# Performance work log

Measured on AMD Instinct MI355X. Metric: run time of the kernel, lower is better.

The kernel has to match this reference:

```python
import jax, jax.numpy as jnp
import numpy as np

B, S, D = 8, 2048, 1024

def setup_inputs() -> dict:
    key = jax.random.key(0)
    ks = jax.random.split(key, 9)
    s = 1.0 / np.sqrt(D)
    return {
        "x": jax.random.normal(ks[0], (B, S, D), dtype=jnp.float32),
        "Wq": jax.random.uniform(ks[1], (D, D), jnp.float32, -s, s),
        "bq": jax.random.uniform(ks[2], (D,), jnp.float32, -s, s),
        "Wk": jax.random.uniform(ks[3], (D, D), jnp.float32, -s, s),
        "bk": jax.random.uniform(ks[4], (D,), jnp.float32, -s, s),
        "Wv": jax.random.uniform(ks[5], (D, D), jnp.float32, -s, s),
        "bv": jax.random.uniform(ks[6], (D,), jnp.float32, -s, s),
        "Wo": jax.random.uniform(ks[7], (D, 1), jnp.float32, -s, s),
        "bo": jax.random.uniform(ks[8], (1,), jnp.float32, -s, s),
    }

def reference(x, Wq, bq, Wk, bk, Wv, bv, Wo, bo):
    q = x @ Wq + bq                      # [B,S,D]
    k = x @ Wk + bk                      # [B,S,D]
    v = x @ Wv + bv                      # [B,S,D]
    scores = jnp.einsum('bsd,btd->bst', q, k)   # [B,S,S], NOTE: no 1/sqrt(D) scaling in source
    attn = jax.nn.softmax(scores, axis=-1)
    out = jnp.einsum('bst,btd->bsd', attn, v)   # [B,S,D]
    return out @ Wo + bo                 # [B,S,1]
```

## Files before the change

### kernel.cpp

```cpp
#include <hip/hip_runtime.h>
#include <stdint.h>

#define D_ 1024
#define S_ 2048
#define B_ 8

typedef _Float16 h16;
typedef _Float16 f16x8 __attribute__((ext_vector_type(8)));
typedef _Float16 f16x4 __attribute__((ext_vector_type(4)));
typedef float    f32x4 __attribute__((ext_vector_type(4)));

typedef __attribute__((address_space(3))) void lds_void;
typedef const __attribute__((address_space(1))) void g_void;

#define MFMA16(a, b, c) __builtin_amdgcn_mfma_f32_16x16x32_f16(a, b, c, 0, 0, 0)
#define VMCNT(n) asm volatile("s_waitcnt vmcnt(" #n ")" ::: "memory")
#define SFENCE() __builtin_amdgcn_sched_barrier(0)
#define SBAR() __builtin_amdgcn_s_barrier()

__device__ __forceinline__ void stage16(const h16* g0, int ld, h16* lchunk) {
  int lane = threadIdx.x & 63;
  int c = (lane & 3) ^ ((lane >> 3) & 3);
  const h16* ga = g0 + (size_t)(lane >> 2) * ld + c * 8;
  __builtin_amdgcn_global_load_lds((g_void*)ga, (lds_void*)lchunk, 16, 0, 0);
}

__global__ void k_cast(const float* __restrict__ Wq, const float* __restrict__ Wk,
                       h16* __restrict__ Wqh, h16* __restrict__ Wkh) {
  int i = blockIdx.x * 256 + threadIdx.x;
  const int n4 = (D_ * D_) / 4;
  const float4* src;
  h16* dst;
  if (i < n4) { src = (const float4*)Wq; dst = Wqh; }
  else        { src = (const float4*)Wk; dst = Wkh; i -= n4; }
  float4 a = src[i];
  f16x4 o;
  o[0] = (h16)a.x; o[1] = (h16)a.y; o[2] = (h16)a.z; o[3] = (h16)a.w;
  *(f16x4*)(dst + (size_t)i * 4) = o;
}

__global__ void k_u(const float* __restrict__ Wv, const float* __restrict__ Wk,
                    const float* __restrict__ Wo, const float* __restrict__ bq_,
                    const float* __restrict__ bv, float* __restrict__ u,
                    float* __restrict__ v2) {
  int lane = threadIdx.x & 63;
  if (blockIdx.x == 256) {
    if (threadIdx.x < 64) {
      float s = 0.f;
      #pragma unroll
      for (int j = 0; j < 4; ++j) {
        float4 a = ((const float4*)bv)[j * 64 + lane];
        float4 b = ((const float4*)Wo)[j * 64 + lane];
        s += a.x * b.x + a.y * b.y + a.z * b.z + a.w * b.w;
      }
      #pragma unroll
      for (int off = 32; off; off >>= 1) s += __shfl_xor(s, off, 64);
      if (lane == 0) u[D_] = s;
    }
    return;
  }
  int row = blockIdx.x * 4 + (threadIdx.x >> 6);
  const float4* rv = (const float4*)(Wv + (size_t)row * D_);
  const float4* rk = (const float4*)(Wk + (size_t)row * D_);
  const float4* w4 = (const float4*)Wo;
  const float4* b4 = (const float4*)bq_;
  float s1 = 0.f, s2 = 0.f;
  #pragma unroll
  for (int j = 0; j < 4; ++j) {
    int c = j * 64 + lane;
    float4 a = rv[c], b = w4[c];
    s1 += a.x * b.x + a.y * b.y + a.z * b.z + a.w * b.w;
    float4 e = rk[c], f = b4[c];
    s2 += e.x * f.x + e.y * f.y + e.z * f.z + e.w * f.w;
  }
  #pragma unroll
  for (int off = 32; off; off >>= 1) {
    s1 += __shfl_xor(s1, off, 64);
    s2 += __shfl_xor(s2, off, 64);
  }
  if (lane == 0) { u[row] = s1; v2[row] = s2; }
}

__global__ void k_xw(const float* __restrict__ x, const float* __restrict__ u,
                     const float* __restrict__ v2, h16* __restrict__ xh,
                     float* __restrict__ w, float* __restrict__ cv) {
  int row = blockIdx.x * 4 + (threadIdx.x >> 6);
  int lane = threadIdx.x & 63;
  const float4* xr = (const float4*)(x + (size_t)row * D_);
  const float4* u4 = (const float4*)u;
  const float4* c4 = (const float4*)v2;
  h16* xo = xh + (size_t)row * D_;
  float s1 = 0.f, s2 = 0.f;
  #pragma unroll
  for (int j = 0; j < 4; ++j) {
    int c = j * 64 + lane;
    float4 a = xr[c];
    float4 b = u4[c];
    float4 e = c4[c];
    s1 += a.x * b.x + a.y * b.y + a.z * b.z + a.w * b.w;
    s2 += a.x * e.x + a.y * e.y + a.z * e.z + a.w * e.w;
    f16x4 o;
    o[0] = (h16)a.x; o[1] = (h16)a.y; o[2] = (h16)a.z; o[3] = (h16)a.w;
    *(f16x4*)(xo + c * 4) = o;
  }
  #pragma unroll
  for (int off = 32; off; off >>= 1) {
    s1 += __shfl_xor(s1, off, 64);
    s2 += __shfl_xor(s2, off, 64);
  }
  if (lane == 0) { w[row] = s1 + u[D_]; cv[row] = s2; }
}

__global__ __launch_bounds__(256, 4) void k_mt(
    const h16* __restrict__ Wkh, const h16* __restrict__ Wqh,
    h16* __restrict__ Mt) {
  __shared__ alignas(16) h16 As[3][128 * 32];
  __shared__ alignas(16) h16 Bs[3][128 * 32];
  int tid = threadIdx.x;
  int w = tid >> 6, lane = tid & 63;
  int wr = w >> 1, wc = w & 1;
  int g = lane >> 4, l15 = lane & 15;
  int swz = (l15 >> 1) & 3;
  int m0 = (blockIdx.x >> 3) * 128, n0 = (blockIdx.x & 7) * 128;

  const h16* abase0 = Wkh + (size_t)(m0 + (2 * w) * 16) * D_;
  const h16* abase1 = abase0 + (size_t)16 * D_;
  const h16* bbase0 = Wqh + (size_t)(n0 + (2 * w) * 16) * D_;
  const h16* bbase1 = bbase0 + (size_t)16 * D_;

  f32x4 acc[4][4] = {};

  #define STAGE_MT(ap, bp, k)                                \
    {                                                        \
      int k0_ = (k) * 32;                                    \
      stage16(abase0 + k0_, D_, (ap) + (2 * w) * 512);       \
      stage16(abase1 + k0_, D_, (ap) + (2 * w + 1) * 512);   \
      stage16(bbase0 + k0_, D_, (bp) + (2 * w) * 512);       \
      stage16(bbase1 + k0_, D_, (bp) + (2 * w + 1) * 512);   \
    }

  h16 *A0 = As[0], *A1 = As[1], *A2 = As[2];
  h16 *B0 = Bs[0], *B1 = Bs[1], *B2 = Bs[2];
  STAGE_MT(A0, B0, 0);
  STAGE_MT(A1, B1, 1);
  for (int k = 0; k < 32; ++k) {
    if (k + 2 < 32) {
      STAGE_MT(A2, B2, k + 2);
      VMCNT(8);
    } else if (k + 1 < 32) {
      VMCNT(4);
    } else {
      VMCNT(0);
    }
    SFENCE();
    SBAR();
    SFENCE();
    f16x8 af[4], bf[4];
    #pragma unroll
    for (int i = 0; i < 4; ++i) {
      af[i] = *(const f16x8*)(A0 + (wr * 64 + i * 16 + l15) * 32 + (g ^ swz) * 8);
      bf[i] = *(const f16x8*)(B0 + (wc * 64 + i * 16 + l15) * 32 + (g ^ swz) * 8);
    }
    __builtin_amdgcn_s_setprio(1);
    #pragma unroll
    for (int mi = 0; mi < 4; ++mi)
      #pragma unroll
      for (int ni = 0; ni < 4; ++ni)
        acc[mi][ni] = MFMA16(af[mi], bf[ni], acc[mi][ni]);
    __builtin_amdgcn_s_setprio(0);
    SBAR();
    h16* t;
    t = A0; A0 = A1; A1 = A2; A2 = t;
    t = B0; B0 = B1; B1 = B2; B2 = t;
  }

  #pragma unroll
  for (int ni = 0; ni < 4; ++ni) {
    int n = n0 + wc * 64 + ni * 16 + l15;
    #pragma unroll
    for (int mi = 0; mi < 4; ++mi) {
      #pragma unroll
      for (int r = 0; r < 4; ++r) {
        int m = m0 + wr * 64 + mi * 16 + g * 4 + r;
        Mt[(size_t)m * D_ + n] = (h16)(acc[mi][ni][r]);
      }
    }
  }
}

__global__ __launch_bounds__(512, 4) void k_y(
    const h16* __restrict__ xh, const h16* __restrict__ Mt,
    h16* __restrict__ y) {
  __shared__ alignas(16) h16 As[3][256 * 32];
  __shared__ alignas(16) h16 Bs[3][128 * 32];
  int tid = threadIdx.x;
  int w = tid >> 6, lane = tid & 63;
  int wrow = w >> 1, wcol = w & 1;
  int g = lane >> 4, l15 = lane & 15;
  int swz = (l15 >> 1) & 3;

  int idx = (blockIdx.x & 7) * 64 + (blockIdx.x >> 3);
  int m0 = (idx >> 3) * 256, n0 = (idx & 7) * 128;

  const h16* abase0 = xh + (size_t)(m0 + (2 * w) * 16) * D_;
  const h16* abase1 = abase0 + (size_t)16 * D_;
  const h16* bbase  = Mt + (size_t)(n0 + w * 16) * D_;

  f32x4 acc[4][4] = {};

  #define STAGE_Y(ap, bp, k)                                 \
    {                                                        \
      int k0_ = (k) * 32;                                    \
      stage16(abase0 + k0_, D_, (ap) + (2 * w) * 512);       \
      stage16(abase1 + k0_, D_, (ap) + (2 * w + 1) * 512);   \
      stage16(bbase + k0_, D_, (bp) + w * 512);              \
    }

  h16 *A0 = As[0], *A1 = As[1], *A2 = As[2];
  h16 *B0 = Bs[0], *B1 = Bs[1], *B2 = Bs[2];
  STAGE_Y(A0, B0, 0);
  STAGE_Y(A1, B1, 1);
  for (int k = 0; k < 32; ++k) {
    if (k + 2 < 32) {
      STAGE_Y(A2, B2, k + 2);
      VMCNT(6);
    } else if (k + 1 < 32) {
      VMCNT(3);
    } else {
      VMCNT(0);
    }
    SFENCE();
    SBAR();
    SFENCE();
    f16x8 af[4], bf[4];
    #pragma unroll
    for (int i = 0; i < 4; ++i) {
      af[i] = *(const f16x8*)(A0 + (wrow * 64 + i * 16 + l15) * 32 + (g ^ swz) * 8);
      bf[i] = *(const f16x8*)(B0 + (wcol * 64 + i * 16 + l15) * 32 + (g ^ swz) * 8);
    }
    __builtin_amdgcn_s_setprio(1);
    #pragma unroll
    for (int mi = 0; mi < 4; ++mi)
      #pragma unroll
      for (int ni = 0; ni < 4; ++ni)
        acc[mi][ni] = MFMA16(af[mi], bf[ni], acc[mi][ni]);
    __builtin_amdgcn_s_setprio(0);
    SBAR();
    h16* t;
    t = A0; A0 = A1; A1 = A2; A2 = t;
    t = B0; B0 = B1; B1 = B2; B2 = t;
  }

  #pragma unroll
  for (int ni = 0; ni < 4; ++ni) {
    int n = n0 + wcol * 64 + ni * 16 + l15;
    #pragma unroll
    for (int mi = 0; mi < 4; ++mi) {
      #pragma unroll
      for (int r = 0; r < 4; ++r) {
        int m = m0 + wrow * 64 + mi * 16 + g * 4 + r;
        y[(size_t)m * D_ + n] = (h16)(acc[mi][ni][r]);
      }
    }
  }
}

__global__ __launch_bounds__(512, 4) void k_attn(
    const h16* __restrict__ y, const h16* __restrict__ xh,
    const float* __restrict__ wv, const float* __restrict__ cv,
    float* __restrict__ part) {
  __shared__ alignas(16) h16 Qs[3][128 * 32];
  __shared__ alignas(16) h16 Ks[3][256 * 32];
  __shared__ float sm[3][4][128];
  int tid = threadIdx.x;
  int w = tid >> 6, lane = tid & 63;
  int g = lane >> 4, l15 = lane & 15;
  int swz = (l15 >> 1) & 3;
  int wq = w >> 2, wkc = w & 3;
  int b = blockIdx.x & 7;
  int r = blockIdx.x >> 3;
  int kc = r >> 4;
  int q0 = (r & 15) * 128;
  size_t rbase = (size_t)b * S_;

  const h16* qbase  = y + (rbase + q0 + w * 16) * D_;
  const h16* kbase0 = xh + (rbase + kc * 256 + (2 * w) * 16) * D_;
  const h16* kbase1 = kbase0 + (size_t)16 * D_;

  #define STAGE_ATTN(qp, kp, st)                             \
    {                                                        \
      int k0_ = (st) * 32;                                   \
      stage16(qbase + k0_, D_, (qp) + w * 512);              \
      stage16(kbase0 + k0_, D_, (kp) + (2 * w) * 512);       \
      stage16(kbase1 + k0_, D_, (kp) + (2 * w + 1) * 512);   \
    }

  f32x4 acc[4][4] = {};

  h16 *Q0 = Qs[0], *Q1 = Qs[1], *Q2 = Qs[2];
  h16 *K0 = Ks[0], *K1 = Ks[1], *K2 = Ks[2];
  STAGE_ATTN(Q0, K0, 0);
  STAGE_ATTN(Q1, K1, 1);
  for (int st = 0; st < 32; ++st) {
    if (st + 2 < 32) {
      STAGE_ATTN(Q2, K2, st + 2);
      VMCNT(6);
    } else if (st + 1 < 32) {
      VMCNT(3);
    } else {
      VMCNT(0);
    }
    SFENCE();
    SBAR();
    SFENCE();
    f16x8 qf[4], kf[4];
    #pragma unroll
    for (int i = 0; i < 4; ++i) {
      qf[i] = *(const f16x8*)(Q0 + (wq * 64 + i * 16 + l15) * 32 + (g ^ swz) * 8);
      kf[i] = *(const f16x8*)(K0 + (wkc * 64 + i * 16 + l15) * 32 + (g ^ swz) * 8);
    }
    __builtin_amdgcn_s_setprio(1);
    #pragma unroll
    for (int mi = 0; mi < 4; ++mi)
      #pragma unroll
      for (int ni = 0; ni < 4; ++ni)
        acc[mi][ni] = MFMA16(qf[mi], kf[ni], acc[mi][ni]);
    __builtin_amdgcn_s_setprio(0);
    SBAR();
    h16* t;
    t = Q0; Q0 = Q1; Q1 = Q2; Q2 = t;
    t = K0; K0 = K1; K1 = K2; K2 = t;
  }

  float wvv[4], cvv[4];
  #pragma unroll
  for (int ni = 0; ni < 4; ++ni) {
    size_t t = rbase + kc * 256 + wkc * 64 + ni * 16 + l15;
    wvv[ni] = wv[t];
    cvv[ni] = cv[t];
  }
  #pragma unroll
  for (int mi = 0; mi < 4; ++mi) {
    #pragma unroll
    for (int rr = 0; rr < 4; ++rr) {
      float s0 = acc[mi][0][rr] + cvv[0];
      float s1 = acc[mi][1][rr] + cvv[1];
      float s2 = acc[mi][2][rr] + cvv[2];
      float s3 = acc[mi][3][rr] + cvv[3];
      float v = fmaxf(fmaxf(s0, s1), fmaxf(s2, s3));
      #pragma unroll
      for (int off = 1; off < 16; off <<= 1) v = fmaxf(v, __shfl_xor(v, off, 64));
      float p0 = __expf(s0 - v), p1 = __expf(s1 - v);
      float p2 = __expf(s2 - v), p3 = __expf(s3 - v);
      float pn = p0 * wvv[0] + p1 * wvv[1] + p2 * wvv[2] + p3 * wvv[3];
      float pd = p0 + p1 + p2 + p3;
      #pragma unroll
      for (int off = 1; off < 16; off <<= 1) {
        pn += __shfl_xor(pn, off, 64);
        pd += __shfl_xor(pd, off, 64);
      }
      if (l15 == 0) {
        int row = wq * 64 + mi * 16 + g * 4 + rr;
        sm[0][wkc][row] = v;
        sm[1][wkc][row] = pn;
        sm[2][wkc][row] = pd;
      }
    }
  }
  __syncthreads();
  if (tid < 128) {
    float M = sm[0][0][tid];
    #pragma unroll
    for (int j = 1; j < 4; ++j) M = fmaxf(M, sm[0][j][tid]);
    float N = 0.f, Dn = 0.f;
    #pragma unroll
    for (int j = 0; j < 4; ++j) {
      float e = __expf(sm[0][j][tid] - M);
      N += sm[1][j][tid] * e;
      Dn += sm[2][j][tid] * e;
    }
    size_t row = rbase + q0 + tid;
    part[row * 24 + kc * 3 + 0] = M;
    part[row * 24 + kc * 3 + 1] = N;
    part[row * 24 + kc * 3 + 2] = Dn;
  }
}

__global__ void k_fin(const float* __restrict__ part, const float* __restrict__ bo,
                      float* __restrict__ out) {
  int idx = blockIdx.x * 256 + threadIdx.x;
  if (idx >= B_ * S_) return;
  const float* p = part + (size_t)idx * 24;
  float M = p[0];
  #pragma unroll
  for (int j = 1; j < 8; ++j) M = fmaxf(M, p[j * 3]);
  float N = 0.f, Dn = 0.f;
  #pragma unroll
  for (int j = 0; j < 8; ++j) {
    float e = __expf(p[j * 3] - M);
    N += p[j * 3 + 1] * e;
    Dn += p[j * 3 + 2] * e;
  }
  out[idx] = N / Dn + bo[0];
}

extern "C" void kernel_launch(void* const* d_in, const int* in_sizes, int n_in,
                              void* d_out, int out_size, void* d_ws, size_t ws_size,
                              hipStream_t stream) {
  const float* x  = (const float*)d_in[0];
  const float* Wq = (const float*)d_in[1];
  const float* bq = (const float*)d_in[2];
  const float* Wk = (const float*)d_in[3];
  const float* bk = (const float*)d_in[4];
  const float* Wv = (const float*)d_in[5];
  const float* bv = (const float*)d_in[6];
  const float* Wo = (const float*)d_in[7];
  const float* bo = (const float*)d_in[8];
  float* out = (float*)d_out;
  (void)bk;

  char* ws = (char*)d_ws;
  h16*   xh   = (h16*)ws;
  h16*   yb   = (h16*)(ws + (size_t)32 * 1024 * 1024);
  h16*   Mt   = (h16*)(ws + (size_t)64 * 1024 * 1024);
  h16*   Wqh  = (h16*)(ws + (size_t)66 * 1024 * 1024);
  h16*   Wkh  = (h16*)(ws + (size_t)68 * 1024 * 1024);
  float* wv   = (float*)(ws + (size_t)70 * 1024 * 1024);
  float* cv   = (float*)(ws + (size_t)70 * 1024 * 1024 + 65536);
  float* u    = (float*)(ws + (size_t)70 * 1024 * 1024 + 131072);
  float* v2   = (float*)(ws + (size_t)70 * 1024 * 1024 + 139264);
  float* part = (float*)(ws + (size_t)71 * 1024 * 1024);

  hipLaunchKernelGGL(k_cast, dim3(2048), dim3(256), 0, stream, Wq, Wk, Wqh, Wkh);
  hipLaunchKernelGGL(k_u,    dim3(257),  dim3(256), 0, stream, Wv, Wk, Wo, bq, bv, u, v2);
  hipLaunchKernelGGL(k_xw,   dim3(4096), dim3(256), 0, stream, x, u, v2, xh, wv, cv);
  hipLaunchKernelGGL(k_mt,   dim3(64),   dim3(256), 0, stream, Wkh, Wqh, Mt);
  hipLaunchKernelGGL(k_y,    dim3(512),  dim3(512), 0, stream, xh, Mt, yb);
  hipLaunchKernelGGL(k_attn, dim3(1024), dim3(512), 0, stream, yb, xh, wv, cv, part);
  hipLaunchKernelGGL(k_fin,  dim3(64),   dim3(256), 0, stream, part, bo, out);
}
```

Baseline: 269.0 us.

## Enlarge GEMM tiles to 256x256 in y and attention-score kernels

Both the y-projection GEMM and the attention score GEMM move from 256x128 (128x256) block tiles to 256x256 tiles. Each wave now computes 128x64 with 8x4 MFMA accumulators, and grid sizes are halved. The aim is higher arithmetic intensity, fewer global and LDS loads per flop, and fewer blocks. The cost is more registers and LDS per block, with launch bounds lowered to 2 blocks per CU, which reduces occupancy and tail-wave balance across 256 CUs.

New measurement: 286.5 us. +6.5%, slower.

```diff
diff --git a/kernel.cpp b/kernel.cpp
--- a/kernel.cpp
+++ b/kernel.cpp
@@ -188,32 +188,34 @@
   }
 }
 
-__global__ __launch_bounds__(512, 4) void k_y(
+__global__ __launch_bounds__(512, 2) void k_y(
     const h16* __restrict__ xh, const h16* __restrict__ Mt,
     h16* __restrict__ y) {
   __shared__ alignas(16) h16 As[3][256 * 32];
-  __shared__ alignas(16) h16 Bs[3][128 * 32];
+  __shared__ alignas(16) h16 Bs[3][256 * 32];
   int tid = threadIdx.x;
   int w = tid >> 6, lane = tid & 63;
-  int wrow = w >> 1, wcol = w & 1;
+  int wq = w >> 2, wn = w & 3;
   int g = lane >> 4, l15 = lane & 15;
   int swz = (l15 >> 1) & 3;
 
-  int idx = (blockIdx.x & 7) * 64 + (blockIdx.x >> 3);
-  int m0 = (idx >> 3) * 256, n0 = (idx & 7) * 128;
+  int idx = (blockIdx.x & 7) * 32 + (blockIdx.x >> 3);
+  int m0 = (idx >> 2) * 256, n0 = (idx & 3) * 256;
 
   const h16* abase0 = xh + (size_t)(m0 + (2 * w) * 16) * D_;
   const h16* abase1 = abase0 + (size_t)16 * D_;
-  const h16* bbase  = Mt + (size_t)(n0 + w * 16) * D_;
-
-  f32x4 acc[4][4] = {};
+  const h16* bbase0 = Mt + (size_t)(n0 + (2 * w) * 16) * D_;
+  const h16* bbase1 = bbase0 + (size_t)16 * D_;
+
+  f32x4 acc[8][4] = {};
 
   #define STAGE_Y(ap, bp, k)                                 \
     {                                                        \
       int k0_ = (k) * 32;                                    \
       stage16(abase0 + k0_, D_, (ap) + (2 * w) * 512);       \
       stage16(abase1 + k0_, D_, (ap) + (2 * w + 1) * 512);   \
-      stage16(bbase + k0_, D_, (bp) + w * 512);              \
+      stage16(bbase0 + k0_, D_, (bp) + (2 * w) * 512);       \
+      stage16(bbase1 + k0_, D_, (bp) + (2 * w + 1) * 512);   \
     }
 
   h16 *A0 = As[0], *A1 = As[1], *A2 = As[2];
@@ -223,24 +225,25 @@
   for (int k = 0; k < 32; ++k) {
     if (k + 2 < 32) {
       STAGE_Y(A2, B2, k + 2);
-      VMCNT(6);
+      VMCNT(8);
     } else if (k + 1 < 32) {
-      VMCNT(3);
+      VMCNT(4);
     } else {
       VMCNT(0);
     }
     SFENCE();
     SBAR();
     SFENCE();
-    f16x8 af[4], bf[4];
-    #pragma unroll
-    for (int i = 0; i < 4; ++i) {
-      af[i] = *(const f16x8*)(A0 + (wrow * 64 + i * 16 + l15) * 32 + (g ^ swz) * 8);
-      bf[i] = *(const f16x8*)(B0 + (wcol * 64 + i * 16 + l15) * 32 + (g ^ swz) * 8);
-    }
+    f16x8 af[8], bf[4];
+    #pragma unroll
+    for (int i = 0; i < 8; ++i)
+      af[i] = *(const f16x8*)(A0 + (wq * 128 + i * 16 + l15) * 32 + (g ^ swz) * 8);
+    #pragma unroll
+    for (int i = 0; i < 4; ++i)
+      bf[i] = *(const f16x8*)(B0 + (wn * 64 + i * 16 + l15) * 32 + (g ^ swz) * 8);
     __builtin_amdgcn_s_setprio(1);
     #pragma unroll
-    for (int mi = 0; mi < 4; ++mi)
+    for (int mi = 0; mi < 8; ++mi)
       #pragma unroll
       for (int ni = 0; ni < 4; ++ni)
         acc[mi][ni] = MFMA16(af[mi], bf[ni], acc[mi][ni]);
@@ -253,25 +256,25 @@
 
   #pragma unroll
   for (int ni = 0; ni < 4; ++ni) {
-    int n = n0 + wcol * 64 + ni * 16 + l15;
-    #pragma unroll
-    for (int mi = 0; mi < 4; ++mi) {
+    int n = n0 + wn * 64 + ni * 16 + l15;
+    #pragma unroll
+    for (int mi = 0; mi < 8; ++mi) {
       #pragma unroll
       for (int r = 0; r < 4; ++r) {
-        int m = m0 + wrow * 64 + mi * 16 + g * 4 + r;
+        int m = m0 + wq * 128 + mi * 16 + g * 4 + r;
         y[(size_t)m * D_ + n] = (h16)(acc[mi][ni][r]);
       }
     }
   }
 }
 
-__global__ __launch_bounds__(512, 4) void k_attn(
+__global__ __launch_bounds__(512, 2) void k_attn(
     const h16* __restrict__ y, const h16* __restrict__ xh,
     const float* __restrict__ wv, const float* __restrict__ cv,
     float* __restrict__ part) {
-  __shared__ alignas(16) h16 Qs[3][128 * 32];
+  __shared__ alignas(16) h16 Qs[3][256 * 32];
   __shared__ alignas(16) h16 Ks[3][256 * 32];
-  __shared__ float sm[3][4][128];
+  __shared__ float sm[3][4][256];
   int tid = threadIdx.x;
   int w = tid >> 6, lane = tid & 63;
   int g = lane >> 4, l15 = lane & 15;
@@ -279,23 +282,25 @@
   int wq = w >> 2, wkc = w & 3;
   int b = blockIdx.x & 7;
   int r = blockIdx.x >> 3;
-  int kc = r >> 4;
-  int q0 = (r & 15) * 128;
+  int kc = r >> 3;
+  int q0 = (r & 7) * 256;
   size_t rbase = (size_t)b * S_;
 
-  const h16* qbase  = y + (rbase + q0 + w * 16) * D_;
+  const h16* qbase0 = y + (rbase + q0 + (2 * w) * 16) * D_;
+  const h16* qbase1 = qbase0 + (size_t)16 * D_;
   const h16* kbase0 = xh + (rbase + kc * 256 + (2 * w) * 16) * D_;
   const h16* kbase1 = kbase0 + (size_t)16 * D_;
 
   #define STAGE_ATTN(qp, kp, st)                             \
     {                                                        \
       int k0_ = (st) * 32;                                   \
-      stage16(qbase + k0_, D_, (qp) + w * 512);              \
+      stage16(qbase0 + k0_, D_, (qp) + (2 * w) * 512);       \
+      stage16(qbase1 + k0_, D_, (qp) + (2 * w + 1) * 512);   \
       stage16(kbase0 + k0_, D_, (kp) + (2 * w) * 512);       \
       stage16(kbase1 + k0_, D_, (kp) + (2 * w + 1) * 512);   \
     }
 
-  f32x4 acc[4][4] = {};
+  f32x4 acc[8][4] = {};
 
   h16 *Q0 = Qs[0], *Q1 = Qs[1], *Q2 = Qs[2];
   h16 *K0 = Ks[0], *K1 = Ks[1], *K2 = Ks[2];
@@ -304,24 +309,25 @@
   for (int st = 0; st < 32; ++st) {
     if (st + 2 < 32) {
       STAGE_ATTN(Q2, K2, st + 2);
-      VMCNT(6);
+      VMCNT(8);
     } else if (st + 1 < 32) {
-      VMCNT(3);
+      VMCNT(4);
     } else {
       VMCNT(0);
     }
     SFENCE();
     SBAR();
     SFENCE();
-    f16x8 qf[4], kf[4];
-    #pragma unroll
-    for (int i = 0; i < 4; ++i) {
-      qf[i] = *(const f16x8*)(Q0 + (wq * 64 + i * 16 + l15) * 32 + (g ^ swz) * 8);
+    f16x8 qf[8], kf[4];
+    #pragma unroll
+    for (int i = 0; i < 8; ++i)
+      qf[i] = *(const f16x8*)(Q0 + (wq * 128 + i * 16 + l15) * 32 + (g ^ swz) * 8);
+    #pragma unroll
+    for (int i = 0; i < 4; ++i)
       kf[i] = *(const f16x8*)(K0 + (wkc * 64 + i * 16 + l15) * 32 + (g ^ swz) * 8);
-    }
     __builtin_amdgcn_s_setprio(1);
     #pragma unroll
-    for (int mi = 0; mi < 4; ++mi)
+    for (int mi = 0; mi < 8; ++mi)
       #pragma unroll
       for (int ni = 0; ni < 4; ++ni)
         acc[mi][ni] = MFMA16(qf[mi], kf[ni], acc[mi][ni]);
@@ -340,7 +346,7 @@
     cvv[ni] = cv[t];
   }
   #pragma unroll
-  for (int mi = 0; mi < 4; ++mi) {
+  for (int mi = 0; mi < 8; ++mi) {
     #pragma unroll
     for (int rr = 0; rr < 4; ++rr) {
       float s0 = acc[mi][0][rr] + cvv[0];
@@ -360,7 +366,7 @@
         pd += __shfl_xor(pd, off, 64);
       }
       if (l15 == 0) {
-        int row = wq * 64 + mi * 16 + g * 4 + rr;
+        int row = wq * 128 + mi * 16 + g * 4 + rr;
         sm[0][wkc][row] = v;
         sm[1][wkc][row] = pn;
         sm[2][wkc][row] = pd;
@@ -368,7 +374,7 @@
     }
   }
   __syncthreads();
-  if (tid < 128) {
+  if (tid < 256) {
     float M = sm[0][0][tid];
     #pragma unroll
     for (int j = 1; j < 4; ++j) M = fmaxf(M, sm[0][j][tid]);
@@ -435,7 +441,7 @@
   hipLaunchKernelGGL(k_u,    dim3(257),  dim3(256), 0, stream, Wv, Wk, Wo, bq, bv, u, v2);
   hipLaunchKernelGGL(k_xw,   dim3(4096), dim3(256), 0, stream, x, u, v2, xh, wv, cv);
   hipLaunchKernelGGL(k_mt,   dim3(64),   dim3(256), 0, stream, Wkh, Wqh, Mt);
-  hipLaunchKernelGGL(k_y,    dim3(512),  dim3(512), 0, stream, xh, Mt, yb);
-  hipLaunchKernelGGL(k_attn, dim3(1024), dim3(512), 0, stream, yb, xh, wv, cv, part);
+  hipLaunchKernelGGL(k_y,    dim3(256),  dim3(512), 0, stream, xh, Mt, yb);
+  hipLaunchKernelGGL(k_attn, dim3(512),  dim3(512), 0, stream, yb, xh, wv, cv, part);
   hipLaunchKernelGGL(k_fin,  dim3(64),   dim3(256), 0, stream, part, bo, out);
 }
```
